# Optimization experiments

Hardware: AMD Instinct MI355X
Metric: run time of the kernel (lower is better)

The kernel has to match this reference:

```python
import jax, jax.numpy as jnp
import numpy as np

B, C, H, W = 8, 256, 32, 32
N, COND_DIM, KV_DIM, REL_DIM = 512, 512, 512, 64
N_HEADS = 8
D_HEAD = KV_DIM // N_HEADS
K_SEL = int(N * 0.6)  # auto mode, shallow layer (layer_idx=2 < total_layers//2=4) -> centrality, ratio_shallow=0.6
NEG = -1e9


def _linear_params(key, fan_in, fan_out):
    kw, kb = jax.random.split(key)
    w = jax.random.normal(kw, (fan_out, fan_in), dtype=jnp.float32) / np.sqrt(fan_in)
    b = jax.random.normal(kb, (fan_out,), dtype=jnp.float32) * 0.01
    return w, b


def _normalize(x, axis=-1):
    # torch F.normalize: x / max(||x||_2, eps)
    n = jnp.sqrt(jnp.sum(x * x, axis=axis, keepdims=True))
    return x / jnp.maximum(n, 1e-12)


def setup_inputs() -> dict:
    key = jax.random.key(0)
    ks = jax.random.split(key, 10)
    h = jax.random.normal(ks[0], (B, C, H, W), dtype=jnp.float32)
    cond_feats = jax.random.normal(ks[1], (B, N, COND_DIM), dtype=jnp.float32)
    cond_mask = jax.random.randint(ks[2], (B, N), 0, 2) > 0  # bool, 1 valid
    Wq, bq = _linear_params(ks[3], C, KV_DIM)
    Wk, bk = _linear_params(ks[4], COND_DIM, KV_DIM)
    Wv, bv = _linear_params(ks[5], COND_DIM, KV_DIM)
    Wrq, brq = _linear_params(ks[6], C, REL_DIM)
    Wrk, brk = _linear_params(ks[7], COND_DIM, REL_DIM)
    Wo, bo = _linear_params(ks[8], KV_DIM, C)
    return dict(h=h, cond_feats=cond_feats, cond_mask=cond_mask,
                Wq=Wq, bq=bq, Wk=Wk, bk=bk, Wv=Wv, bv=bv,
                Wrq=Wrq, brq=brq, Wrk=Wrk, brk=brk, Wo=Wo, bo=bo)


def reference(h, cond_feats, cond_mask, Wq, bq, Wk, bk, Wv, bv, Wrq, brq, Wrk, brk, Wo, bo):
    Bq, Ch, Hh, Ww = h.shape
    S = Hh * Ww
    # ---- q/k/v projections ----
    q = h.reshape(Bq, Ch, S).transpose(0, 2, 1)                # (B,S,C)
    q = q @ Wq.T + bq                                           # (B,S,KV)
    K = cond_feats @ Wk.T + bk                                  # (B,N,KV)
    V = cond_feats @ Wv.T + bv
    qh = q.reshape(Bq, S, N_HEADS, D_HEAD).transpose(0, 2, 1, 3)
    kh = K.reshape(Bq, N, N_HEADS, D_HEAD).transpose(0, 2, 1, 3)
    vh = V.reshape(Bq, N, N_HEADS, D_HEAD).transpose(0, 2, 1, 3)
    attn_scores = jnp.einsum('bhqd,bhkd->bhqk', qh, kh) / np.sqrt(D_HEAD)
    # ---- selector: auto mode, shallow -> centrality scores ----
    qg = h.mean(axis=(2, 3))                                    # adaptive_avg_pool2d(h,1) -> (B,C)
    qg_proj = _normalize(qg @ Wrq.T + brq)                      # (B,REL)  (unused branch kept faithful)
    cond_proj = _normalize(cond_feats @ Wrk.T + brk)            # (B,N,REL)
    Smat = jnp.einsum('bnd,bmd->bnm', cond_proj, cond_proj)     # (B,N,N)
    eye = jnp.eye(N, dtype=bool)
    centrality = jnp.where(eye[None], 0.0, Smat).sum(axis=-1)   # (B,N)
    scores = centrality
    # ---- top-k mask via scatter ----
    topk_idx = jax.lax.top_k(scores, K_SEL)[1]                  # (B,K)
    selected = jnp.zeros((Bq, N), dtype=bool).at[jnp.arange(Bq)[:, None], topk_idx].set(True)
    allowed = selected & cond_mask
    rows_all_false = ~allowed.any(axis=1)                       # (B,)
    idx0 = jnp.argmax(scores, axis=-1)                          # top-1 fallback
    fallback = jax.nn.one_hot(idx0, N, dtype=bool)
    allowed = allowed | (rows_all_false[:, None] & fallback)
    attn_scores = jnp.where(allowed[:, None, None, :], attn_scores, NEG)
    # ---- attention ----
    attn = jax.nn.softmax(attn_scores, axis=-1)
    out = jnp.einsum('bhqk,bhkd->bhqd', attn, vh)               # (B,h,S,d)
    out = out.transpose(0, 2, 1, 3).reshape(Bq, S, KV_DIM)
    out = out @ Wo.T + bo                                       # (B,S,C)
    return out.transpose(0, 2, 1).reshape(Bq, Ch, Hh, Ww)
```

## Files before the change

### kernel.cpp

```cpp
#include <hip/hip_runtime.h>
#include <math.h>

#define B_ 8
#define C_ 256
#define S_ 1024
#define N_ 512
#define KV_ 512
#define REL_ 64
#define NH_ 8
#define DH_ 64
#define KSEL_ 307

typedef __attribute__((ext_vector_type(8))) short bf16x8;
typedef __attribute__((ext_vector_type(4))) short short4v;
typedef __attribute__((ext_vector_type(4))) float f32x4;

__device__ __forceinline__ short f2bf(float f) {
  unsigned int u = __float_as_uint(f);
  u += 0x7fffu + ((u >> 16) & 1u);
  return (short)(u >> 16);
}

__global__ __launch_bounds__(256) void k_prep(const float* __restrict__ cond, const float* __restrict__ Wq,
                                              const float* __restrict__ Wk, const float* __restrict__ Wv,
                                              const float* __restrict__ Wo, const float* __restrict__ h,
                                              const float* __restrict__ Wrk,
                                              short* __restrict__ cond_b, short* __restrict__ Wq_b,
                                              short* __restrict__ Wk_b, short* __restrict__ Wv_b,
                                              short* __restrict__ Wo_b, short* __restrict__ hT,
                                              float* __restrict__ cp_part) {
  __shared__ float fs[4160];
  int blk = blockIdx.x, tid = threadIdx.x;
  if (blk < 256) {
    int bm = (blk & 63) * 64, kb = blk >> 6;
    float* As = fs;
    float* Bs = fs + 1088;
    int tm = (tid >> 4) << 2, tn = (tid & 15) << 2;
    float acc[4][4] = {};
    for (int k0 = kb * 128; k0 < kb * 128 + 128; k0 += 16) {
      #pragma unroll
      for (int ii = 0; ii < 4; ++ii) {
        int idx = tid + ii * 256;
        int r = idx >> 4, k = idx & 15;
        As[r * 17 + k] = cond[(size_t)(bm + r) * KV_ + k0 + k];
        Bs[r * 17 + k] = Wrk[(size_t)r * KV_ + k0 + k];
      }
      __syncthreads();
      #pragma unroll
      for (int k = 0; k < 16; ++k) {
        float a[4], bb[4];
        #pragma unroll
        for (int x = 0; x < 4; ++x) { a[x] = As[(tm + x) * 17 + k]; bb[x] = Bs[(tn + x) * 17 + k]; }
        #pragma unroll
        for (int x = 0; x < 4; ++x)
          #pragma unroll
          for (int y = 0; y < 4; ++y)
            acc[x][y] += a[x] * bb[y];
      }
      __syncthreads();
    }
    #pragma unroll
    for (int x = 0; x < 4; ++x)
      #pragma unroll
      for (int y = 0; y < 4; ++y)
        cp_part[(size_t)kb * 262144 + (size_t)(bm + tm + x) * 64 + tn + y] = acc[x][y];
  } else if (blk < 768) {
    int i = blk - 256;
    int s0 = (i & 15) * 64, c0 = ((i >> 4) & 3) * 64, b = i >> 6;
    int x = tid & 63, y0 = tid >> 6;
    #pragma unroll
    for (int y = y0; y < 64; y += 4)
      fs[y * 65 + x] = h[((size_t)(b * C_ + c0 + y)) * S_ + s0 + x];
    __syncthreads();
    #pragma unroll
    for (int y = y0; y < 64; y += 4)
      hT[((size_t)(b * S_ + s0 + y)) * C_ + c0 + x] = f2bf(fs[x * 65 + y]);
  } else {
    int base = blk - 768;
    const float* src; short* dst;
    if (base < 1024)      { src = cond; dst = cond_b; }
    else if (base < 1088) { src = Wq;   dst = Wq_b;   base -= 1024; }
    else if (base < 1216) { src = Wk;   dst = Wk_b;   base -= 1088; }
    else if (base < 1344) { src = Wv;   dst = Wv_b;   base -= 1216; }
    else                  { src = Wo;   dst = Wo_b;   base -= 1344; }
    int j = base * 256 + tid;
    float4 v0 = ((const float4*)src)[j * 2];
    float4 v1 = ((const float4*)src)[j * 2 + 1];
    bf16x8 o = { f2bf(v0.x), f2bf(v0.y), f2bf(v0.z), f2bf(v0.w),
                 f2bf(v1.x), f2bf(v1.y), f2bf(v1.z), f2bf(v1.w) };
    ((bf16x8*)dst)[j] = o;
  }
}

__global__ __launch_bounds__(256) void k_normalize(const float* __restrict__ cp_part, const float* __restrict__ brk,
                                                   float* __restrict__ cp) {
  int row = blockIdx.x * 4 + (threadIdx.x >> 6);
  int d = threadIdx.x & 63;
  size_t off = (size_t)row * 64 + d;
  float x = brk[d];
  #pragma unroll
  for (int s = 0; s < 4; ++s) x += cp_part[(size_t)s * 262144 + off];
  float ss = x * x;
  #pragma unroll
  for (int o = 32; o; o >>= 1) ss += __shfl_xor(ss, o);
  cp[off] = x / fmaxf(sqrtf(ss), 1e-12f);
}

__global__ __launch_bounds__(512) void k_select(const float* __restrict__ cp, const int* __restrict__ mask,
                                                int* __restrict__ idxb, int* __restrict__ cnt) {
  int b = blockIdx.x, tid = threadIdx.x;
  __shared__ float part[8][64];
  __shared__ float vsum[64];
  __shared__ float sc[512];
  __shared__ int wcnt[8];
  int d = tid & 63, g = tid >> 6;
  float sacc = 0.f;
  for (int n = g * 64; n < g * 64 + 64; ++n)
    sacc += cp[((size_t)b * N_ + n) * 64 + d];
  part[g][d] = sacc;
  __syncthreads();
  if (tid < 64) {
    float v = 0.f;
    #pragma unroll
    for (int gg = 0; gg < 8; ++gg) v += part[gg][tid];
    vsum[tid] = v;
  }
  __syncthreads();
  const float* x = cp + ((size_t)b * N_ + tid) * 64;
  float dsum = 0.f, dself = 0.f;
  #pragma unroll
  for (int dd = 0; dd < 64; ++dd) {
    float xv = x[dd];
    dsum += xv * vsum[dd];
    dself += xv * xv;
  }
  sc[tid] = dsum - dself;
  __syncthreads();
  float v = sc[tid];
  int rank = 0;
  for (int j = 0; j < N_; ++j) {
    float u = sc[j];
    rank += (u > v) || (u == v && j < tid);
  }
  int sel = (rank < KSEL_) && (mask[b * N_ + tid] != 0);
  unsigned long long bal = __ballot(sel);
  if ((tid & 63) == 0) wcnt[g] = __popcll(bal);
  __syncthreads();
  int off2 = 0, total = 0;
  #pragma unroll
  for (int i = 0; i < 8; ++i) { int c = wcnt[i]; total += c; if (i < g) off2 += c; }
  int pos = off2 + __popcll(bal & ((1ull << (tid & 63)) - 1ull));
  if (sel) idxb[b * N_ + pos] = tid;
  if (total == 0 && rank == 0) idxb[b * N_] = tid;
  if (tid == 0) cnt[b] = (total == 0) ? 1 : total;
}

template<int MODE, int GA, int GB, int WM>
__device__ __forceinline__ void gemm_body(const short* __restrict__ A, const short* __restrict__ W,
                                          const float* __restrict__ bias, void* __restrict__ Cout,
                                          short* As, short* Bs, size_t bm, size_t bn, int Kd, int Nout,
                                          const int* __restrict__ gidx, int cntv) {
  constexpr int BMv = WM * 32;
  constexpr int NIA = BMv / 64;
  constexpr int OPS = NIA + 2;
  int tid = threadIdx.x;
  int lane = tid & 63, wid = tid >> 6;
  int wr = wid >> 1, wc = wid & 1;
  f32x4 acc[WM][4] = {};
  int srow = lane >> 2;
  int schunk = lane & 3;
  int steps = Kd >> 5;

  int rowA[NIA ? NIA : 1], rowB[2];
  #pragma unroll
  for (int i = 0; i < NIA; ++i) {
    int rt = wid * (WM * 8) + i * 16 + srow;
    rowA[i] = GA ? (((int)bm + rt < cntv) ? gidx[bm + rt] : 0) : (int)(bm + rt);
  }
  #pragma unroll
  for (int i = 0; i < 2; ++i) {
    int rt = wid * 32 + i * 16 + srow;
    rowB[i] = GB ? (((int)bn + rt < cntv) ? gidx[bn + rt] : 0) : (int)(bn + rt);
  }

  #define STAGE_G(t, buf)                                                                              \
    {                                                                                                  \
      int k0s = (t) * 32;                                                                              \
      _Pragma("unroll")                                                                                \
      for (int i = 0; i < NIA; ++i) {                                                                  \
        int rt = wid * (WM * 8) + i * 16 + srow;                                                       \
        int sc_ = (schunk ^ ((rt >> 1) & 3)) * 8;                                                      \
        const short* ga = A + (size_t)rowA[i] * Kd + k0s + sc_;                                        \
        __builtin_amdgcn_global_load_lds((const __attribute__((address_space(1))) void*)ga,            \
            (__attribute__((address_space(3))) void*)(As + (buf) * (BMv * 32) +                        \
                                                     (wid * (WM * 8) + i * 16) * 32),                  \
            16, 0, 0);                                                                                 \
      }                                                                                                \
      _Pragma("unroll")                                                                                \
      for (int i = 0; i < 2; ++i) {                                                                    \
        int rt = wid * 32 + i * 16 + srow;                                                             \
        int sc_ = (schunk ^ ((rt >> 1) & 3)) * 8;                                                      \
        const short* gb = W + (size_t)rowB[i] * Kd + k0s + sc_;                                        \
        __builtin_amdgcn_global_load_lds((const __attribute__((address_space(1))) void*)gb,            \
            (__attribute__((address_space(3))) void*)(Bs + (buf) * 4096 + (wid * 32 + i * 16) * 32),   \
            16, 0, 0);                                                                                 \
      }                                                                                                \
    }

  STAGE_G(0, 0);
  STAGE_G(1, 1);

  int cur = 0;
  for (int t = 0; t < steps; ++t) {
    if (t == steps - 1)
      asm volatile("s_waitcnt vmcnt(0)" ::: "memory");
    else
      asm volatile("s_waitcnt vmcnt(%0)" :: "n"(OPS) : "memory");
    __syncthreads();
    if (t + 2 < steps) {
      int nb = cur + 2; if (nb >= 3) nb -= 3;
      STAGE_G(t + 2, nb);
    }
    const short* Ac = As + cur * (BMv * 32);
    const short* Bc = Bs + cur * 4096;
    bf16x8 a[WM], b[4];
    #pragma unroll
    for (int m = 0; m < WM; ++m) {
      int rt = wr * (WM * 16) + m * 16 + (lane & 15);
      a[m] = *(const bf16x8*)(Ac + rt * 32 + (((lane >> 4) ^ ((rt >> 1) & 3)) * 8));
    }
    #pragma unroll
    for (int n = 0; n < 4; ++n) {
      int rt = wc * 64 + n * 16 + (lane & 15);
      b[n] = *(const bf16x8*)(Bc + rt * 32 + (((lane >> 4) ^ ((rt >> 1) & 3)) * 8));
    }
    #pragma unroll
    for (int m = 0; m < WM; ++m)
      #pragma unroll
      for (int n = 0; n < 4; ++n)
        acc[m][n] = __builtin_amdgcn_mfma_f32_16x16x32_bf16(a[m], b[n], acc[m][n], 0, 0, 0);
    cur = (cur == 2) ? 0 : cur + 1;
  }
  #undef STAGE_G

  int c0 = lane & 15, r0q = lane >> 4;
  #pragma unroll
  for (int n = 0; n < 4; ++n) {
    size_t col = bn + wc * 64 + n * 16 + c0;
    #pragma unroll
    for (int m = 0; m < WM; ++m) {
      #pragma unroll
      for (int j = 0; j < 4; ++j) {
        size_t row = bm + wr * (WM * 16) + m * 16 + r0q * 4 + j;
        if (MODE == 0) {
          ((short*)Cout)[row * Nout + col] = f2bf(acc[m][n][j] + bias[col]);
        } else if (MODE == 1) {
          ((float*)Cout)[((col >> 10) * C_ + row) * S_ + (col & (S_ - 1))] = acc[m][n][j] + bias[row];
        } else {
          ((short*)Cout)[row * Nout + col] = f2bf(acc[m][n][j] + bias[row]);
        }
      }
    }
  }
}

__global__ __launch_bounds__(256) void k_fused_proj(const short* __restrict__ hT, const short* __restrict__ cond_b,
                                                    const short* __restrict__ Wq_b, const short* __restrict__ Wk_b,
                                                    const short* __restrict__ Wv_b,
                                                    const float* __restrict__ bq, const float* __restrict__ bk,
                                                    const float* __restrict__ bv,
                                                    short* __restrict__ qb, short* __restrict__ Kc,
                                                    short* __restrict__ Vtc,
                                                    const int* __restrict__ idxb, const int* __restrict__ cnt) {
  __shared__ short smem[24576];
  int blk = blockIdx.x;
  if (blk < 192) {
    int b = blk / 24, j = blk % 24;
    int mt = j >> 2, ntile = j & 3;
    int cv = cnt[b], padded = (cv + 63) & ~63;
    if (mt * 64 >= padded) return;
    gemm_body<0, 1, 0, 2>(cond_b + (size_t)b * N_ * KV_, Wk_b, bk, Kc + (size_t)b * N_ * KV_,
                          smem, smem + 12288, (size_t)mt * 64, (size_t)ntile * 128, KV_, KV_,
                          idxb + b * N_, cv);
  } else if (blk < 384) {
    int i = blk - 192, b = i / 24, j = i % 24;
    int ntc = j >> 3, mtd = j & 7;
    int cv = cnt[b], padded = (cv + 63) & ~63;
    if (ntc * 128 >= padded) return;
    gemm_body<3, 0, 1, 2>(Wv_b, cond_b + (size_t)b * N_ * KV_, bv, Vtc + (size_t)b * 512 * N_,
                          smem, smem + 12288, (size_t)mtd * 64, (size_t)ntc * 128, KV_, N_,
                          idxb + b * N_, cv);
  } else {
    int i = blk - 384;
    gemm_body<0, 0, 0, 4>(hT, Wq_b, bq, qb, smem, smem + 12288,
                          (size_t)(i & 63) * 128, (size_t)(i >> 6) * 128, C_, KV_, nullptr, 0);
  }
}

__device__ __forceinline__ void stage_tile64_w8(const short* gRowBase, int gStride, short* ldsBase, int wid, int lane) {
  int sub = lane >> 3;
  int colE = ((lane & 7) ^ sub) * 8;
  int r = wid * 8 + sub;
  const short* gp = gRowBase + (size_t)r * gStride + colE;
  __builtin_amdgcn_global_load_lds((const __attribute__((address_space(1))) void*)gp,
                                   (__attribute__((address_space(3))) void*)(ldsBase + wid * 512),
                                   16, 0, 0);
}

#define QK2L 0.18033688f
__global__ __launch_bounds__(512) void k_attn_mfma(const short* __restrict__ qb, const short* __restrict__ Kc,
                                                   const short* __restrict__ Vtc, const int* __restrict__ cnt,
                                                   short* __restrict__ attn_b) {
  __shared__ short Ps[8192];
  __shared__ short Ks[2][4096];
  __shared__ short Vs[2][4096];
  int g = blockIdx.x;
  int xcd = g & 7, li = g >> 3;
  int bh = xcd * 8 + (li >> 3);
  int qt = li & 7;
  int b = bh >> 3, h = bh & 7;
  int tid = threadIdx.x, lane = tid & 63, wid = tid >> 6;
  int hi = lane >> 4, q = lane & 15;
  int swz = (lane & 7) << 3;
  int s0 = qt * 128;
  int cntv = cnt[b];
  int nt = (cntv + 63) >> 6;
  const short* Qg = qb + ((size_t)(b * S_ + s0) * KV_ + h * DH_);
  const short* Kg = Kc + ((size_t)(b * N_) * KV_ + h * DH_);
  const short* Vg = Vtc + ((size_t)((b * NH_ + h) * DH_) * N_);

  bf16x8 qf0 = *(const bf16x8*)(Qg + (size_t)(wid * 16 + q) * KV_ + hi * 8);
  bf16x8 qf1 = *(const bf16x8*)(Qg + (size_t)(wid * 16 + q) * KV_ + 32 + hi * 8);

  stage_tile64_w8(Kg, KV_, Ks[0], wid, lane);
  stage_tile64_w8(Vg, N_, Vs[0], wid, lane);
  asm volatile("s_waitcnt vmcnt(0)" ::: "memory");
  __syncthreads();

  float m = -1e30f, l = 0.f;
  f32x4 o[4] = {};

  for (int t = 0; t < nt; ++t) {
    int cur = t & 1;
    const short* Kcur = Ks[cur];
    const short* Vcur = Vs[cur];
    if (t + 1 < nt) {
      stage_tile64_w8(Kg + (size_t)(t + 1) * 64 * KV_, KV_, Ks[cur ^ 1], wid, lane);
      stage_tile64_w8(Vg + (t + 1) * 64, N_, Vs[cur ^ 1], wid, lane);
    }
    f32x4 pv[4];
    __builtin_amdgcn_s_setprio(1);
    #pragma unroll
    for (int kf = 0; kf < 4; ++kf) {
      bf16x8 k0 = *(const bf16x8*)&Kcur[(kf * 16 + q) * 64 + ((hi * 8) ^ swz)];
      bf16x8 k1 = *(const bf16x8*)&Kcur[(kf * 16 + q) * 64 + ((32 + hi * 8) ^ swz)];
      f32x4 z = {0.f, 0.f, 0.f, 0.f};
      pv[kf] = __builtin_amdgcn_mfma_f32_16x16x32_bf16(k0, qf0, z, 0, 0, 0);
      pv[kf] = __builtin_amdgcn_mfma_f32_16x16x32_bf16(k1, qf1, pv[kf], 0, 0, 0);
    }
    __builtin_amdgcn_s_setprio(0);
    float sv[16];
    int kbase = t * 64 + hi * 4;
    #pragma unroll
    for (int kf = 0; kf < 4; ++kf) {
      #pragma unroll
      for (int r = 0; r < 4; ++r)
        sv[kf * 4 + r] = (kbase + kf * 16 + r < cntv) ? pv[kf][r] * QK2L : -1e30f;
    }
    float tmax = sv[0];
    #pragma unroll
    for (int i = 1; i < 16; ++i) tmax = fmaxf(tmax, sv[i]);
    tmax = fmaxf(tmax, __shfl_xor(tmax, 16));
    tmax = fmaxf(tmax, __shfl_xor(tmax, 32));
    float mnew = fmaxf(m, tmax);
    float scale = exp2f(m - mnew);
    float psum = 0.f;
    #pragma unroll
    for (int i = 0; i < 16; ++i) { sv[i] = exp2f(sv[i] - mnew); psum += sv[i]; }
    psum += __shfl_xor(psum, 16);
    psum += __shfl_xor(psum, 32);
    l = l * scale + psum;
    m = mnew;
    #pragma unroll
    for (int df = 0; df < 4; ++df) {
      o[df][0] *= scale; o[df][1] *= scale; o[df][2] *= scale; o[df][3] *= scale;
    }
    int pbase = wid * 1024 + q * 64;
    #pragma unroll
    for (int kf = 0; kf < 4; ++kf) {
      short4v pk = { f2bf(sv[kf * 4 + 0]), f2bf(sv[kf * 4 + 1]), f2bf(sv[kf * 4 + 2]), f2bf(sv[kf * 4 + 3]) };
      *(short4v*)&Ps[pbase + ((kf * 16 + hi * 4) ^ swz)] = pk;
    }
    __builtin_amdgcn_s_setprio(1);
    #pragma unroll
    for (int ks = 0; ks < 2; ++ks) {
      bf16x8 pb = *(const bf16x8*)&Ps[pbase + ((ks * 32 + hi * 8) ^ swz)];
      #pragma unroll
      for (int df = 0; df < 4; ++df) {
        bf16x8 vf = *(const bf16x8*)&Vcur[(df * 16 + q) * 64 + ((ks * 32 + hi * 8) ^ swz)];
        o[df] = __builtin_amdgcn_mfma_f32_16x16x32_bf16(vf, pb, o[df], 0, 0, 0);
      }
    }
    __builtin_amdgcn_s_setprio(0);
    if (t + 1 < nt) {
      asm volatile("s_waitcnt vmcnt(0)" ::: "memory");
      __syncthreads();
    }
  }
  float inv = 1.0f / l;
  short* op = attn_b + ((size_t)(b * S_ + s0 + wid * 16 + q) * KV_ + h * DH_);
  #pragma unroll
  for (int df = 0; df < 4; ++df) {
    short4v ov = { f2bf(o[df][0] * inv), f2bf(o[df][1] * inv), f2bf(o[df][2] * inv), f2bf(o[df][3] * inv) };
    *(short4v*)&op[df * 16 + hi * 4] = ov;
  }
}

__global__ __launch_bounds__(256) void k_outproj(const short* __restrict__ Wo_b, const short* __restrict__ attn_b,
                                                 const float* __restrict__ bo, float* __restrict__ out) {
  __shared__ short smem[18432];
  int bid = blockIdx.x;
  int xcd = bid & 7, j = bid >> 3;
  int p = ((j >> 2) << 3) | xcd;
  int i = j & 3;
  gemm_body<1, 0, 0, 2>(Wo_b, attn_b, bo, out, smem, smem + 6144,
                        (size_t)i * 64, (size_t)p * 128, KV_, B_ * S_, nullptr, 0);
}

extern "C" void kernel_launch(void* const* d_in, const int* in_sizes, int n_in,
                              void* d_out, int out_size, void* d_ws, size_t ws_size,
                              hipStream_t stream) {
  const float* h         = (const float*)d_in[0];
  const float* cond      = (const float*)d_in[1];
  const int*   cond_mask = (const int*)d_in[2];
  const float* Wq = (const float*)d_in[3];
  const float* bq = (const float*)d_in[4];
  const float* Wk = (const float*)d_in[5];
  const float* bk = (const float*)d_in[6];
  const float* Wv = (const float*)d_in[7];
  const float* bv = (const float*)d_in[8];
  const float* Wrk = (const float*)d_in[11];
  const float* brk = (const float*)d_in[12];
  const float* Wo  = (const float*)d_in[13];
  const float* bo  = (const float*)d_in[14];
  float* out = (float*)d_out;

  char* w = (char*)d_ws;
  short* qb      = (short*)(w + 0);
  short* Kc      = (short*)(w + 8388608);
  short* Vtc     = (short*)(w + 12582912);
  short* attn_b  = (short*)(w + 16777216);
  short* hT      = (short*)(w + 25165824);
  short* cond_b  = (short*)(w + 29360128);
  float* cp_part = (float*)(w + 33554432);
  float* cp      = (float*)(w + 37748736);
  int*   idxb    = (int*)  (w + 38797312);
  int*   cnt     = (int*)  (w + 38813696);
  short* Wq_b    = (short*)(w + 38813760);
  short* Wk_b    = (short*)(w + 39075904);
  short* Wv_b    = (short*)(w + 39600192);
  short* Wo_b    = (short*)(w + 40124480);

  k_prep<<<2176, 256, 0, stream>>>(cond, Wq, Wk, Wv, Wo, h, Wrk,
                                   cond_b, Wq_b, Wk_b, Wv_b, Wo_b, hT, cp_part);
  k_normalize<<<1024, 256, 0, stream>>>(cp_part, brk, cp);
  k_select<<<8, 512, 0, stream>>>(cp, cond_mask, idxb, cnt);
  k_fused_proj<<<640, 256, 0, stream>>>(hT, cond_b, Wq_b, Wk_b, Wv_b, bq, bk, bv,
                                        qb, Kc, Vtc, idxb, cnt);
  k_attn_mfma<<<512, 512, 0, stream>>>(qb, Kc, Vtc, cnt, attn_b);
  k_outproj<<<256, 256, 0, stream>>>(Wo_b, attn_b, bo, out);
}
```

Measured before the change: 88.55 us.

## Fuse relation projection normalization into prep kernel, drop split-K partials

The cond·Wrk^T projection in k_prep is no longer split-K across four blocks with partials written to global memory. Each block now computes 16 full rows over the whole K range, then adds the bias and L2-normalizes in-register with a 16-lane shuffle reduction. This removes the k_normalize launch and the 4 MB partial-buffer round trip. In exchange, each thread computes only 4 outputs instead of 16, and reloads the full 64x16 Wrk tile every k-step, so compute density drops and Wrk is re-read by every block.

```diff
diff --git a/kernel.cpp b/kernel.cpp
--- a/kernel.cpp
+++ b/kernel.cpp
@@ -24,46 +24,50 @@
 __global__ __launch_bounds__(256) void k_prep(const float* __restrict__ cond, const float* __restrict__ Wq,
                                               const float* __restrict__ Wk, const float* __restrict__ Wv,
                                               const float* __restrict__ Wo, const float* __restrict__ h,
-                                              const float* __restrict__ Wrk,
+                                              const float* __restrict__ Wrk, const float* __restrict__ brk,
                                               short* __restrict__ cond_b, short* __restrict__ Wq_b,
                                               short* __restrict__ Wk_b, short* __restrict__ Wv_b,
                                               short* __restrict__ Wo_b, short* __restrict__ hT,
-                                              float* __restrict__ cp_part) {
+                                              float* __restrict__ cp) {
   __shared__ float fs[4160];
   int blk = blockIdx.x, tid = threadIdx.x;
   if (blk < 256) {
-    int bm = (blk & 63) * 64, kb = blk >> 6;
+    int bm = blk * 16;
     float* As = fs;
-    float* Bs = fs + 1088;
-    int tm = (tid >> 4) << 2, tn = (tid & 15) << 2;
-    float acc[4][4] = {};
-    for (int k0 = kb * 128; k0 < kb * 128 + 128; k0 += 16) {
+    float* Bs = fs + 272;
+    int row = tid >> 4;
+    int cgrp = tid & 15;
+    int tn = cgrp * 4;
+    float acc[4] = {};
+    for (int k0 = 0; k0 < KV_; k0 += 16) {
+      As[row * 17 + cgrp] = cond[(size_t)(bm + row) * KV_ + k0 + cgrp];
       #pragma unroll
       for (int ii = 0; ii < 4; ++ii) {
         int idx = tid + ii * 256;
         int r = idx >> 4, k = idx & 15;
-        As[r * 17 + k] = cond[(size_t)(bm + r) * KV_ + k0 + k];
         Bs[r * 17 + k] = Wrk[(size_t)r * KV_ + k0 + k];
       }
       __syncthreads();
       #pragma unroll
       for (int k = 0; k < 16; ++k) {
-        float a[4], bb[4];
+        float a = As[row * 17 + k];
         #pragma unroll
-        for (int x = 0; x < 4; ++x) { a[x] = As[(tm + x) * 17 + k]; bb[x] = Bs[(tn + x) * 17 + k]; }
-        #pragma unroll
-        for (int x = 0; x < 4; ++x)
-          #pragma unroll
-          for (int y = 0; y < 4; ++y)
-            acc[x][y] += a[x] * bb[y];
+        for (int y = 0; y < 4; ++y)
+          acc[y] += a * Bs[(tn + y) * 17 + k];
       }
       __syncthreads();
     }
-    #pragma unroll
-    for (int x = 0; x < 4; ++x)
-      #pragma unroll
-      for (int y = 0; y < 4; ++y)
-        cp_part[(size_t)kb * 262144 + (size_t)(bm + tm + x) * 64 + tn + y] = acc[x][y];
+    float ss = 0.f;
+    #pragma unroll
+    for (int y = 0; y < 4; ++y) {
+      acc[y] += brk[tn + y];
+      ss += acc[y] * acc[y];
+    }
+    #pragma unroll
+    for (int o = 1; o < 16; o <<= 1) ss += __shfl_xor(ss, o);
+    float rinv = 1.0f / fmaxf(sqrtf(ss), 1e-12f);
+    float4 ov = { acc[0] * rinv, acc[1] * rinv, acc[2] * rinv, acc[3] * rinv };
+    *(float4*)&cp[(size_t)(bm + row) * 64 + tn] = ov;
   } else if (blk < 768) {
     int i = blk - 256;
     int s0 = (i & 15) * 64, c0 = ((i >> 4) & 3) * 64, b = i >> 6;
@@ -90,20 +94,6 @@
                  f2bf(v1.x), f2bf(v1.y), f2bf(v1.z), f2bf(v1.w) };
     ((bf16x8*)dst)[j] = o;
   }
-}
-
-__global__ __launch_bounds__(256) void k_normalize(const float* __restrict__ cp_part, const float* __restrict__ brk,
-                                                   float* __restrict__ cp) {
-  int row = blockIdx.x * 4 + (threadIdx.x >> 6);
-  int d = threadIdx.x & 63;
-  size_t off = (size_t)row * 64 + d;
-  float x = brk[d];
-  #pragma unroll
-  for (int s = 0; s < 4; ++s) x += cp_part[(size_t)s * 262144 + off];
-  float ss = x * x;
-  #pragma unroll
-  for (int o = 32; o; o >>= 1) ss += __shfl_xor(ss, o);
-  cp[off] = x / fmaxf(sqrtf(ss), 1e-12f);
 }
 
 __global__ __launch_bounds__(512) void k_select(const float* __restrict__ cp, const int* __restrict__ mask,
@@ -452,18 +442,16 @@
   short* attn_b  = (short*)(w + 16777216);
   short* hT      = (short*)(w + 25165824);
   short* cond_b  = (short*)(w + 29360128);
-  float* cp_part = (float*)(w + 33554432);
-  float* cp      = (float*)(w + 37748736);
-  int*   idxb    = (int*)  (w + 38797312);
-  int*   cnt     = (int*)  (w + 38813696);
-  short* Wq_b    = (short*)(w + 38813760);
-  short* Wk_b    = (short*)(w + 39075904);
-  short* Wv_b    = (short*)(w + 39600192);
-  short* Wo_b    = (short*)(w + 40124480);
-
-  k_prep<<<2176, 256, 0, stream>>>(cond, Wq, Wk, Wv, Wo, h, Wrk,
-                                   cond_b, Wq_b, Wk_b, Wv_b, Wo_b, hT, cp_part);
-  k_normalize<<<1024, 256, 0, stream>>>(cp_part, brk, cp);
+  float* cp      = (float*)(w + 33554432);
+  int*   idxb    = (int*)  (w + 34603008);
+  int*   cnt     = (int*)  (w + 34619392);
+  short* Wq_b    = (short*)(w + 34619456);
+  short* Wk_b    = (short*)(w + 34881600);
+  short* Wv_b    = (short*)(w + 35405888);
+  short* Wo_b    = (short*)(w + 35930176);
+
+  k_prep<<<2176, 256, 0, stream>>>(cond, Wq, Wk, Wv, Wo, h, Wrk, brk,
+                                   cond_b, Wq_b, Wk_b, Wv_b, Wo_b, hT, cp);
   k_select<<<8, 512, 0, stream>>>(cp, cond_mask, idxb, cnt);
   k_fused_proj<<<640, 256, 0, stream>>>(hT, cond_b, Wq_b, Wk_b, Wv_b, bq, bk, bv,
                                         qb, Kc, Vtc, idxb, cnt);
```

After: 101.3 us. +14.4%, slower.
